# Kernel tuning notes

Measured on AMD Instinct MI355X. Metric: run time of the kernel, lower is better.

## Reference

```python
import jax, jax.numpy as jnp
import numpy as np


def setup_inputs() -> dict:
    key = jax.random.key(0)
    k1, k2, k3, k4, k5 = jax.random.split(key, 5)
    B, C, G, H, W = 2, 64, 4, 64, 64
    CG = C * G            # 256 complex input channels (flattened)
    DQK = max(C // 8, 1)  # 8  query/key channels after gabor pooling
    scale = 1.0 / np.sqrt(CG)
    x = jax.random.normal(k1, (2, B, C, G, H, W), dtype=jnp.float32)
    wq = jax.random.normal(k2, (2, DQK, CG), dtype=jnp.float32) * scale
    wk = jax.random.normal(k3, (2, DQK, CG), dtype=jnp.float32) * scale
    wv = jax.random.normal(k4, (2, CG, CG), dtype=jnp.float32) * scale
    gamma = jax.random.normal(k5, (1,), dtype=jnp.float32) * 0.1
    return {"x": x, "wq": wq, "wk": wk, "wv": wv, "gamma": gamma}


def _cconv1x1(w, xr, xi):
    """Complex 1x1 conv: (wr+i wi)(xr+i xi). w: (2,O,Cin), x: (B,Cin,L)."""
    wr, wi = w[0], w[1]
    yr = jnp.einsum('oc,bcl->bol', wr, xr) - jnp.einsum('oc,bcl->bol', wi, xi)
    yi = jnp.einsum('oc,bcl->bol', wr, xi) + jnp.einsum('oc,bcl->bol', wi, xr)
    return yr, yi


def reference(x, wq, wk, wv, gamma):
    _, B, C, G, H, W = x.shape
    L = H * W
    xr = x[0].reshape(B, C * G, L)
    xi = x[1].reshape(B, C * G, L)
    # complex Q (B,d,L) / K (B,d,L)
    qr, qi = _cconv1x1(wq, xr, xi)
    kr, ki = _cconv1x1(wk, xr, xi)
    # energy = Q^H-free complex bmm: energy[b,l,m] = sum_d q[b,d,l] * k[b,d,m]
    er = jnp.einsum('bdl,bdm->blm', qr, kr) - jnp.einsum('bdl,bdm->blm', qi, ki)
    ei = jnp.einsum('bdl,bdm->blm', qr, ki) + jnp.einsum('bdl,bdm->blm', qi, kr)
    # magnitude-squared softmax over last axis -> real attention (B,L,L)
    att = jax.nn.softmax(er * er + ei * ei, axis=-1)
    # complex V (B,CG,L); out[b,c,m] = sum_l v[b,c,l] * att[b,m,l]
    vr, vi = _cconv1x1(wv, xr, xi)
    out_r = jnp.einsum('bcl,bml->bcm', vr, att)
    out_i = jnp.einsum('bcl,bml->bcm', vi, att)
    out = jnp.stack([out_r, out_i]).reshape(2, B, C, G, H, W)
    return gamma * out + x
```

## Files before the change

### kernel.cpp

```cpp
#include <hip/hip_runtime.h>
#include <cstdint>

constexpr int Bc  = 2;
constexpr int CGc = 256;
constexpr int Dc  = 8;
constexpr int Lc  = 4096;

typedef __attribute__((ext_vector_type(8))) short short8;
typedef __attribute__((ext_vector_type(4))) float floatx4;

__device__ inline unsigned short f2bf(float f) {
  union { float f; unsigned u; } v; v.f = f;
  unsigned r = v.u + 0x7fffu + ((v.u >> 16) & 1u);
  return (unsigned short)(r >> 16);
}
__device__ inline float bf2f(unsigned short h) {
  return __uint_as_float((unsigned)h << 16);
}

__global__ __launch_bounds__(256) void init_wcat(float* __restrict__ stats,
                                                 const float* __restrict__ wv,
                                                 unsigned short* __restrict__ Wcat) {
  const int bx = blockIdx.x;
  if (bx < 64) {
    stats[bx * 256 + threadIdx.x] = 0.f;
    return;
  }
  const int i  = (bx - 64) * 256 + threadIdx.x;
  const int cc = i >> 9, k = i & 511;
  const int co = cc >> 8, c = cc & 255, ci = k >> 8, cin = k & 255;
  const float wr = wv[(size_t)c * CGc + cin];
  const float wi = wv[(size_t)(CGc + c) * CGc + cin];
  const float val = co == 0 ? (ci == 0 ? wr : -wi) : (ci == 0 ? wi : wr);
  Wcat[i] = f2bf(val);
}

__global__ __launch_bounds__(256) void xT_pack(const float* __restrict__ x,
                                               unsigned short* __restrict__ Xlk) {
  __shared__ float xs[64][65];
  const int tid = threadIdx.x;
  const int b   = blockIdx.z;
  const int l0  = blockIdx.x * 64;
  const int c0  = blockIdx.y * 64;
  const int lt  = tid & 63, r4 = tid >> 6;
#pragma unroll
  for (int p = 0; p < 16; ++p) {
    const int row  = p * 4 + r4;
    const int cin2 = c0 + row;
    const int comp = cin2 >> 8, cin = cin2 & 255;
    xs[row][lt] = x[((size_t)(comp * Bc + b) * CGc + cin) * Lc + l0 + lt];
  }
  __syncthreads();
#pragma unroll
  for (int p = 0; p < 16; ++p) {
    const int lr = p * 4 + r4;
    Xlk[((size_t)b * Lc + l0 + lr) * 512 + c0 + lt] = f2bf(xs[lt][lr]);
  }
}

__global__ __launch_bounds__(256) void qk_projpack(const float* __restrict__ x,
                                                   const float* __restrict__ wq,
                                                   const float* __restrict__ wk,
                                                   unsigned short* __restrict__ Qcat,
                                                   unsigned short* __restrict__ K1hi,
                                                   unsigned short* __restrict__ K1lo,
                                                   unsigned short* __restrict__ K2hi,
                                                   unsigned short* __restrict__ K2lo) {
  __shared__ float ws[4 * Dc * CGc];
  __shared__ float qs[32][16];
  __shared__ float ks[32][16];
  const int tid = threadIdx.x;
  const int b   = blockIdx.y;
  for (int i = tid; i < 2 * Dc * CGc; i += 256) {
    ws[i]                 = wq[i];
    ws[2 * Dc * CGc + i]  = wk[i];
  }
  __syncthreads();
  const int d  = tid >> 5;
  const int ml = tid & 31;
  const int m  = blockIdx.x * 32 + ml;
  const float* xr = x + ((size_t)(0 * Bc + b) * CGc) * Lc + m;
  const float* xi = x + ((size_t)(1 * Bc + b) * CGc) * Lc + m;
  const float* wqr = ws + d * CGc;
  const float* wqi = ws + (Dc + d) * CGc;
  const float* wkr = ws + 2 * Dc * CGc + d * CGc;
  const float* wki = ws + 2 * Dc * CGc + (Dc + d) * CGc;
  float qer = 0.f, qei = 0.f, ker = 0.f, kei = 0.f;
#pragma unroll 4
  for (int cin = 0; cin < CGc; ++cin) {
    const float vr = xr[(size_t)cin * Lc];
    const float vi = xi[(size_t)cin * Lc];
    const float a1 = wqr[cin], b1 = wqi[cin];
    qer = fmaf(a1, vr, qer); qer = fmaf(-b1, vi, qer);
    qei = fmaf(a1, vi, qei); qei = fmaf(b1, vr, qei);
    const float a2 = wkr[cin], b2 = wki[cin];
    ker = fmaf(a2, vr, ker); ker = fmaf(-b2, vi, ker);
    kei = fmaf(a2, vi, kei); kei = fmaf(b2, vr, kei);
  }
  qs[ml][d] = qer;  qs[ml][8 + d] = qei;
  ks[ml][d] = ker;  ks[ml][8 + d] = kei;
  __syncthreads();
  const int part = tid >> 5;
  const int rl   = tid & 31;
  const size_t r = (size_t)b * Lc + blockIdx.x * 32 + rl;
  if (part < 2) {
    unsigned u[8];
#pragma unroll
    for (int t = 0; t < 8; ++t) {
      const float v0 = qs[rl][2 * t], v1 = qs[rl][2 * t + 1];
      const unsigned short h0 = f2bf(v0), h1 = f2bf(v1);
      if (part == 0) {
        u[t] = (unsigned)h0 | ((unsigned)h1 << 16);
      } else {
        const unsigned short l0 = f2bf(v0 - bf2f(h0));
        const unsigned short l1 = f2bf(v1 - bf2f(h1));
        u[t] = (unsigned)l0 | ((unsigned)l1 << 16);
      }
    }
    uint4* dst = (uint4*)(Qcat + r * 32 + part * 16);
    dst[0] = make_uint4(u[0], u[1], u[2], u[3]);
    dst[1] = make_uint4(u[4], u[5], u[6], u[7]);
  } else if (part < 6) {
    float kv[16];
    if (part < 4) {
#pragma unroll
      for (int e = 0; e < 8; ++e) { kv[e] = ks[rl][e]; kv[8 + e] = -ks[rl][8 + e]; }
    } else {
#pragma unroll
      for (int e = 0; e < 8; ++e) { kv[e] = ks[rl][8 + e]; kv[8 + e] = ks[rl][e]; }
    }
    const int lo = part & 1;
    unsigned u[8];
#pragma unroll
    for (int t = 0; t < 8; ++t) {
      const unsigned short h0 = f2bf(kv[2 * t]), h1 = f2bf(kv[2 * t + 1]);
      if (!lo) {
        u[t] = (unsigned)h0 | ((unsigned)h1 << 16);
      } else {
        const unsigned short l0 = f2bf(kv[2 * t] - bf2f(h0));
        const unsigned short l1 = f2bf(kv[2 * t + 1] - bf2f(h1));
        u[t] = (unsigned)l0 | ((unsigned)l1 << 16);
      }
    }
    unsigned short* base = part < 4 ? (lo ? K1lo : K1hi) : (lo ? K2lo : K2hi);
    uint4* dst = (uint4*)(base + r * 16);
    dst[0] = make_uint4(u[0], u[1], u[2], u[3]);
    dst[1] = make_uint4(u[4], u[5], u[6], u[7]);
  }
}

__global__ __launch_bounds__(256) void v_gemm(const unsigned short* __restrict__ Wcat,
                                              const unsigned short* __restrict__ Xlk,
                                              unsigned short* __restrict__ vbf) {
  __shared__ short As[128 * 64];
  __shared__ short Bs[64 * 64];
  const int tid  = threadIdx.x;
  const int b    = blockIdx.z;
  const int cc0  = blockIdx.x * 128;
  const int l0   = blockIdx.y * 64;
  const int wid  = tid >> 6, lane = tid & 63;
  const int wcc  = (wid >> 1) * 64;
  const int wl   = (wid & 1) * 32;
  const int lrow = lane & 15, quad = lane >> 4;
  floatx4 acc[4][2] = {};
  const unsigned short* wsrc = Wcat + (size_t)cc0 * 512;
  const unsigned short* xsrc = Xlk + ((size_t)b * Lc + l0) * 512;
  int s_off[4], g_off[4];
#pragma unroll
  for (int r = 0; r < 4; ++r) {
    const int idx = r * 256 + tid;
    const int row = idx >> 3, ch = idx & 7;
    s_off[r] = row * 64 + (ch ^ (row & 7)) * 8;
    g_off[r] = row * 512 + ch * 8;
  }
  short8 ar[4], br[2];
#pragma unroll
  for (int r = 0; r < 4; ++r) ar[r] = *(const short8*)(wsrc + g_off[r]);
#pragma unroll
  for (int r = 0; r < 2; ++r) br[r] = *(const short8*)(xsrc + g_off[r]);
  for (int k0 = 0; k0 < 512; k0 += 64) {
    __syncthreads();
#pragma unroll
    for (int r = 0; r < 4; ++r) *(short8*)&As[s_off[r]] = ar[r];
#pragma unroll
    for (int r = 0; r < 2; ++r) *(short8*)&Bs[s_off[r]] = br[r];
    __syncthreads();
    if (k0 + 64 < 512) {
#pragma unroll
      for (int r = 0; r < 4; ++r) ar[r] = *(const short8*)(wsrc + g_off[r] + k0 + 64);
#pragma unroll
      for (int r = 0; r < 2; ++r) br[r] = *(const short8*)(xsrc + g_off[r] + k0 + 64);
    }
#pragma unroll
    for (int kk = 0; kk < 64; kk += 32) {
      const int cb = kk >> 3;
      short8 af[4], bf[2];
#pragma unroll
      for (int i = 0; i < 4; ++i)
        af[i] = *(const short8*)&As[(wcc + i * 16 + lrow) * 64 +
                                    ((cb + quad) ^ (lrow & 7)) * 8];
#pragma unroll
      for (int j = 0; j < 2; ++j)
        bf[j] = *(const short8*)&Bs[(wl + j * 16 + lrow) * 64 +
                                    ((cb + quad) ^ (lrow & 7)) * 8];
#pragma unroll
      for (int i = 0; i < 4; ++i)
#pragma unroll
        for (int j = 0; j < 2; ++j)
          acc[i][j] = __builtin_amdgcn_mfma_f32_16x16x32_bf16(af[i], bf[j], acc[i][j], 0, 0, 0);
    }
  }
#pragma unroll
  for (int i = 0; i < 4; ++i) {
    const int ccb = cc0 + wcc + i * 16 + quad * 4;
#pragma unroll
    for (int j = 0; j < 2; ++j) {
      const int l = l0 + wl + j * 16 + lrow;
#pragma unroll
      for (int rg = 0; rg < 4; ++rg)
        vbf[((size_t)b * 512 + ccb + rg) * Lc + l] = f2bf(acc[i][j][rg]);
    }
  }
}

__global__ __launch_bounds__(256) void e_max(const unsigned short* __restrict__ Qcat,
                                             const unsigned short* __restrict__ K1hi,
                                             const unsigned short* __restrict__ K2hi,
                                             float* __restrict__ Mrow) {
  const int tid  = threadIdx.x;
  const int w    = tid >> 6, lane = tid & 63;
  const int lrow = lane & 15, quad = lane >> 4, qsel = quad & 1;
  const int b    = blockIdx.z;
  const int m16  = blockIdx.x * 64 + w * 16;
  const int lbeg = blockIdx.y * 512;
  const size_t kb = (size_t)b * Lc;
  const short8 afrag = *(const short8*)(Qcat + (kb + m16 + lrow) * 32 + quad * 8);
  float mx[4] = {0.f, 0.f, 0.f, 0.f};
  for (int l0 = lbeg; l0 < lbeg + 512; l0 += 16) {
    const size_t l = kb + l0 + lrow;
    const short8 b1h = *(const short8*)(K1hi + l * 16 + qsel * 8);
    const short8 b2h = *(const short8*)(K2hi + l * 16 + qsel * 8);
    const floatx4 er = __builtin_amdgcn_mfma_f32_16x16x32_bf16(afrag, b1h, (floatx4){0.f, 0.f, 0.f, 0.f}, 0, 0, 0);
    const floatx4 ei = __builtin_amdgcn_mfma_f32_16x16x32_bf16(afrag, b2h, (floatx4){0.f, 0.f, 0.f, 0.f}, 0, 0, 0);
#pragma unroll
    for (int r = 0; r < 4; ++r) {
      float e = er[r] * er[r];
      e = fmaf(ei[r], ei[r], e);
      mx[r] = fmaxf(mx[r], e);
    }
  }
#pragma unroll
  for (int r = 0; r < 4; ++r) {
    float v = mx[r];
#pragma unroll
    for (int off = 1; off < 16; off <<= 1) v = fmaxf(v, __shfl_xor(v, off));
    if (lrow == 0)
      atomicMax((unsigned*)&Mrow[kb + m16 + quad * 4 + r], __float_as_uint(v));
  }
}

__global__ __launch_bounds__(256) void e_exp(const unsigned short* __restrict__ Qcat,
                                             const unsigned short* __restrict__ K1hi,
                                             const unsigned short* __restrict__ K1lo,
                                             const unsigned short* __restrict__ K2hi,
                                             const unsigned short* __restrict__ K2lo,
                                             const float* __restrict__ Mrow,
                                             unsigned short* __restrict__ att,
                                             float* __restrict__ Ssum) {
  const int tid  = threadIdx.x;
  const int w    = tid >> 6, lane = tid & 63;
  const int lrow = lane & 15, quad = lane >> 4, qsel = quad & 1;
  const int b    = blockIdx.z;
  const int m16  = blockIdx.x * 64 + w * 16;
  const int lbeg = blockIdx.y * 512;
  const size_t kb = (size_t)b * Lc;
  const short8 afrag = *(const short8*)(Qcat + (kb + m16 + lrow) * 32 + quad * 8);
  float Mv[4], sum[4] = {};
#pragma unroll
  for (int r = 0; r < 4; ++r) Mv[r] = Mrow[kb + m16 + quad * 4 + r];
  for (int l0 = lbeg; l0 < lbeg + 512; l0 += 16) {
    const size_t l = kb + l0 + lrow;
    const short8 b1h = *(const short8*)(K1hi + l * 16 + qsel * 8);
    const short8 b1l = *(const short8*)(K1lo + l * 16 + qsel * 8);
    const short8 b2h = *(const short8*)(K2hi + l * 16 + qsel * 8);
    const short8 b2l = *(const short8*)(K2lo + l * 16 + qsel * 8);
    floatx4 er = __builtin_amdgcn_mfma_f32_16x16x32_bf16(afrag, b1l, (floatx4){0.f, 0.f, 0.f, 0.f}, 0, 0, 0);
    er = __builtin_amdgcn_mfma_f32_16x16x32_bf16(afrag, b1h, er, 0, 0, 0);
    floatx4 ei = __builtin_amdgcn_mfma_f32_16x16x32_bf16(afrag, b2l, (floatx4){0.f, 0.f, 0.f, 0.f}, 0, 0, 0);
    ei = __builtin_amdgcn_mfma_f32_16x16x32_bf16(afrag, b2h, ei, 0, 0, 0);
#pragma unroll
    for (int r = 0; r < 4; ++r) {
      float e = er[r] * er[r];
      e = fmaf(ei[r], ei[r], e);
      const float wgt = __expf(e - Mv[r]);
      sum[r] += wgt;
      att[(kb + m16 + quad * 4 + r) * Lc + l0 + lrow] = f2bf(wgt);
    }
  }
#pragma unroll
  for (int r = 0; r < 4; ++r) {
    float v = sum[r];
#pragma unroll
    for (int off = 1; off < 16; off <<= 1) v += __shfl_xor(v, off);
    if (lrow == 0) atomicAdd(&Ssum[kb + m16 + quad * 4 + r], v);
  }
}

__device__ __forceinline__ void pv_stage(const unsigned short* __restrict__ vsrc,
                                         const unsigned short* __restrict__ asrc,
                                         short* lds_buf, int k0, int wid, int lane) {
  const int rsub = lane >> 3;
  const int ch   = (lane & 7) ^ rsub;
#pragma unroll
  for (int t = 0; t < 4; ++t) {
    const int q    = wid * 4 + t;
    const int tile = q >> 4;
    const int j    = q & 15;
    const int row  = j * 8 + rsub;
    const unsigned short* g =
        (tile == 0 ? vsrc : asrc) + (size_t)row * Lc + k0 + ch * 8;
    short* l = lds_buf + tile * 8192 + j * 512;
    __builtin_amdgcn_global_load_lds(
        (const __attribute__((address_space(1))) void*)g,
        (__attribute__((address_space(3))) void*)l, 16, 0, 0);
  }
}

__device__ __forceinline__ void pv_compute32(const short* __restrict__ As,
                                             const short* __restrict__ Bs,
                                             int cb, int wcc, int wm, int lrow, int quad,
                                             floatx4 (&acc)[4][4]) {
  short8 af[4], bf[4];
#pragma unroll
  for (int i = 0; i < 4; ++i)
    af[i] = *(const short8*)&As[(wcc + i * 16 + lrow) * 64 +
                                ((cb + quad) ^ (lrow & 7)) * 8];
#pragma unroll
  for (int j = 0; j < 4; ++j)
    bf[j] = *(const short8*)&Bs[(wm + j * 16 + lrow) * 64 +
                                ((cb + quad) ^ (lrow & 7)) * 8];
#pragma unroll
  for (int i = 0; i < 4; ++i)
#pragma unroll
    for (int j = 0; j < 4; ++j)
      acc[i][j] = __builtin_amdgcn_mfma_f32_16x16x32_bf16(af[i], bf[j], acc[i][j], 0, 0, 0);
}

__global__ __launch_bounds__(512, 2) void pv_gemm(const unsigned short* __restrict__ v,
                                                  const unsigned short* __restrict__ att,
                                                  const float* __restrict__ Ssum,
                                                  const float* __restrict__ x,
                                                  const float* __restrict__ gamma,
                                                  float* __restrict__ out) {
  extern __shared__ short smem[];
  const int flat = blockIdx.x;
  const int swz  = (flat & 7) * 32 + (flat >> 3);
  const int b    = swz >> 7;
  const int rem  = swz & 127;
  const int m0   = (rem >> 2) * 128;
  const int cc0  = (rem & 3) * 128;
  const int tid  = threadIdx.x;
  const int wid  = tid >> 6, lane = tid & 63;
  const int g    = wid >> 2;
  const int w4   = wid & 3;
  const int wcc  = (w4 >> 1) * 64;
  const int wm   = (w4 & 1) * 64;
  const int lrow = lane & 15, quad = lane >> 4;
  const int cb   = g * 4;
  floatx4 acc[4][4] = {};
  const unsigned short* vsrc = v   + ((size_t)b * 512 + cc0) * Lc;
  const unsigned short* asrc = att + ((size_t)b * Lc + m0) * Lc;
  pv_stage(vsrc, asrc, smem,          0, wid, lane);
  pv_stage(vsrc, asrc, smem + 16384, 64, wid, lane);
  int cur = 0;
  for (int p = 0; p < 64; ++p) {
    if (p < 63) {
      asm volatile("s_waitcnt vmcnt(4)" ::: "memory");
    } else {
      asm volatile("s_waitcnt vmcnt(0)" ::: "memory");
    }
    __builtin_amdgcn_s_barrier();
    __builtin_amdgcn_sched_barrier(0);
    if (p + 2 < 64) {
      const int nxt = cur + 2 > 2 ? cur - 1 : cur + 2;
      pv_stage(vsrc, asrc, smem + nxt * 16384, (p + 2) * 64, wid, lane);
    }
    __builtin_amdgcn_sched_barrier(0);
    pv_compute32(smem + cur * 16384, smem + cur * 16384 + 8192,
                 cb, wcc, wm, lrow, quad, acc);
    __builtin_amdgcn_sched_barrier(0);
    cur = cur + 1 > 2 ? 0 : cur + 1;
  }
  __syncthreads();
  float* red = (float*)smem;
  if (g == 1) {
#pragma unroll
    for (int i = 0; i < 4; ++i)
#pragma unroll
      for (int j = 0; j < 4; ++j) {
        const int tq = i * 4 + j;
        *(floatx4*)&red[((w4 * 64 + lane) * 16 + (tq ^ (lane & 15))) * 4] = acc[i][j];
      }
  }
  __syncthreads();
  if (g == 0) {
#pragma unroll
    for (int i = 0; i < 4; ++i)
#pragma unroll
      for (int j = 0; j < 4; ++j) {
        const int tq = i * 4 + j;
        const floatx4 o = *(const floatx4*)&red[((w4 * 64 + lane) * 16 + (tq ^ (lane & 15))) * 4];
        acc[i][j] += o;
      }
    const float gm = gamma[0];
    float svj[4];
#pragma unroll
    for (int j = 0; j < 4; ++j)
      svj[j] = gm / Ssum[(size_t)b * Lc + m0 + wm + j * 16 + lrow];
#pragma unroll
    for (int i = 0; i < 4; ++i) {
      const int ccb = cc0 + wcc + i * 16 + quad * 4;
#pragma unroll
      for (int j = 0; j < 4; ++j) {
        const int m = m0 + wm + j * 16 + lrow;
#pragma unroll
        for (int rg = 0; rg < 4; ++rg) {
          const int cc   = ccb + rg;
          const int comp = cc >> 8, c = cc & 255;
          const size_t idx = (((size_t)comp * Bc + b) * CGc + c) * Lc + m;
          out[idx] = svj[j] * acc[i][j][rg] + x[idx];
        }
      }
    }
  }
}

extern "C" void kernel_launch(void* const* d_in, const int* in_sizes, int n_in,
                              void* d_out, int out_size, void* d_ws, size_t ws_size,
                              hipStream_t stream) {
  const float* x     = (const float*)d_in[0];
  const float* wq    = (const float*)d_in[1];
  const float* wk    = (const float*)d_in[2];
  const float* wv    = (const float*)d_in[3];
  const float* gamma = (const float*)d_in[4];
  float* out = (float*)d_out;

  float* q    = (float*)d_ws;
  float* kk   = q    + (size_t)Bc * Lc * 16;
  float* Mrow = kk   + (size_t)Bc * Lc * 16;
  float* Ssum = Mrow + (size_t)Bc * Lc;
  unsigned short* vbf  = (unsigned short*)(Ssum + (size_t)Bc * Lc);
  unsigned short* att  = vbf + (size_t)Bc * 512 * Lc;
  unsigned short* Xlk  = att;
  unsigned short* Qcat = att + (size_t)Bc * Lc * Lc;
  unsigned short* K1hi = Qcat + (size_t)Bc * Lc * 32;
  unsigned short* K1lo = K1hi + (size_t)Bc * Lc * 16;
  unsigned short* K2hi = K1lo + (size_t)Bc * Lc * 16;
  unsigned short* K2lo = K2hi + (size_t)Bc * Lc * 16;
  unsigned short* Wcat = K2lo + (size_t)Bc * Lc * 16;

  init_wcat<<<dim3(64 + 1024), 256, 0, stream>>>(Mrow, wv, Wcat);
  qk_projpack<<<dim3(Lc / 32, Bc), 256, 0, stream>>>(x, wq, wk, Qcat, K1hi, K1lo, K2hi, K2lo);
  xT_pack<<<dim3(Lc / 64, 8, Bc), 256, 0, stream>>>(x, Xlk);
  v_gemm<<<dim3(512 / 128, Lc / 64, Bc), 256, 0, stream>>>(Wcat, Xlk, vbf);
  e_max<<<dim3(Lc / 64, 8, Bc), 256, 0, stream>>>(Qcat, K1hi, K2hi, Mrow);
  e_exp<<<dim3(Lc / 64, 8, Bc), 256, 0, stream>>>(Qcat, K1hi, K1lo, K2hi, K2lo, Mrow, att, Ssum);
  pv_gemm<<<dim3(256), 512, 3 * 16384 * sizeof(short), stream>>>(vbf, att, Ssum, x, gamma, out);
}
```

Measured before the change: 194.6 us.

## Fuse row-max and exp passes in one block; widen PV GEMM K-tile and split-K

Merges the e_max and e_exp kernels into one 1024-thread kernel where each block owns 32 rows across all L. The row max and row sum are reduced in LDS instead of through global atomics, which removes the stats-zeroing pass and one launch. The PV GEMM moves to 1024 threads per block with 128-wide K tiles and double buffering instead of triple buffering with 64-wide tiles. It also gains a 4-way split-K reduction through LDS. In exchange, occupancy drops to one block per CU and there is less prefetch depth to hide load latency.

```diff
diff --git a/kernel.cpp b/kernel.cpp
--- a/kernel.cpp
+++ b/kernel.cpp
@@ -18,15 +18,9 @@
   return __uint_as_float((unsigned)h << 16);
 }
 
-__global__ __launch_bounds__(256) void init_wcat(float* __restrict__ stats,
-                                                 const float* __restrict__ wv,
+__global__ __launch_bounds__(256) void wcat_pack(const float* __restrict__ wv,
                                                  unsigned short* __restrict__ Wcat) {
-  const int bx = blockIdx.x;
-  if (bx < 64) {
-    stats[bx * 256 + threadIdx.x] = 0.f;
-    return;
-  }
-  const int i  = (bx - 64) * 256 + threadIdx.x;
+  const int i  = blockIdx.x * 256 + threadIdx.x;
   const int cc = i >> 9, k = i & 511;
   const int co = cc >> 8, c = cc & 255, ci = k >> 8, cin = k & 255;
   const float wr = wv[(size_t)c * CGc + cin];
@@ -223,17 +217,26 @@
   }
 }
 
-__global__ __launch_bounds__(256) void e_max(const unsigned short* __restrict__ Qcat,
-                                             const unsigned short* __restrict__ K1hi,
-                                             const unsigned short* __restrict__ K2hi,
-                                             float* __restrict__ Mrow) {
+__global__ __launch_bounds__(1024) void emax_exp(const unsigned short* __restrict__ Qcat,
+                                                 const unsigned short* __restrict__ K1hi,
+                                                 const unsigned short* __restrict__ K1lo,
+                                                 const unsigned short* __restrict__ K2hi,
+                                                 const unsigned short* __restrict__ K2lo,
+                                                 unsigned short* __restrict__ att,
+                                                 float* __restrict__ Ssum) {
+  __shared__ unsigned maxb[32];
+  __shared__ float    sumb[32];
   const int tid  = threadIdx.x;
-  const int w    = tid >> 6, lane = tid & 63;
+  const int wv   = tid >> 6, lane = tid & 63;
   const int lrow = lane & 15, quad = lane >> 4, qsel = quad & 1;
-  const int b    = blockIdx.z;
-  const int m16  = blockIdx.x * 64 + w * 16;
-  const int lbeg = blockIdx.y * 512;
+  const int b    = blockIdx.y;
+  const int rg   = wv & 1;
+  const int sl   = wv >> 1;
+  const int m16  = blockIdx.x * 32 + rg * 16;
+  const int lbeg = sl * 512;
   const size_t kb = (size_t)b * Lc;
+  if (tid < 32) { maxb[tid] = 0u; sumb[tid] = 0.f; }
+  __syncthreads();
   const short8 afrag = *(const short8*)(Qcat + (kb + m16 + lrow) * 32 + quad * 8);
   float mx[4] = {0.f, 0.f, 0.f, 0.f};
   for (int l0 = lbeg; l0 < lbeg + 512; l0 += 16) {
@@ -255,29 +258,12 @@
 #pragma unroll
     for (int off = 1; off < 16; off <<= 1) v = fmaxf(v, __shfl_xor(v, off));
     if (lrow == 0)
-      atomicMax((unsigned*)&Mrow[kb + m16 + quad * 4 + r], __float_as_uint(v));
-  }
-}
-
-__global__ __launch_bounds__(256) void e_exp(const unsigned short* __restrict__ Qcat,
-                                             const unsigned short* __restrict__ K1hi,
-                                             const unsigned short* __restrict__ K1lo,
-                                             const unsigned short* __restrict__ K2hi,
-                                             const unsigned short* __restrict__ K2lo,
-                                             const float* __restrict__ Mrow,
-                                             unsigned short* __restrict__ att,
-                                             float* __restrict__ Ssum) {
-  const int tid  = threadIdx.x;
-  const int w    = tid >> 6, lane = tid & 63;
-  const int lrow = lane & 15, quad = lane >> 4, qsel = quad & 1;
-  const int b    = blockIdx.z;
-  const int m16  = blockIdx.x * 64 + w * 16;
-  const int lbeg = blockIdx.y * 512;
-  const size_t kb = (size_t)b * Lc;
-  const short8 afrag = *(const short8*)(Qcat + (kb + m16 + lrow) * 32 + quad * 8);
+      atomicMax(&maxb[rg * 16 + quad * 4 + r], __float_as_uint(v));
+  }
+  __syncthreads();
   float Mv[4], sum[4] = {};
 #pragma unroll
-  for (int r = 0; r < 4; ++r) Mv[r] = Mrow[kb + m16 + quad * 4 + r];
+  for (int r = 0; r < 4; ++r) Mv[r] = __uint_as_float(maxb[rg * 16 + quad * 4 + r]);
   for (int l0 = lbeg; l0 < lbeg + 512; l0 += 16) {
     const size_t l = kb + l0 + lrow;
     const short8 b1h = *(const short8*)(K1hi + l * 16 + qsel * 8);
@@ -302,42 +288,45 @@
     float v = sum[r];
 #pragma unroll
     for (int off = 1; off < 16; off <<= 1) v += __shfl_xor(v, off);
-    if (lrow == 0) atomicAdd(&Ssum[kb + m16 + quad * 4 + r], v);
-  }
-}
-
-__device__ __forceinline__ void pv_stage(const unsigned short* __restrict__ vsrc,
-                                         const unsigned short* __restrict__ asrc,
-                                         short* lds_buf, int k0, int wid, int lane) {
-  const int rsub = lane >> 3;
-  const int ch   = (lane & 7) ^ rsub;
+    if (lrow == 0) atomicAdd(&sumb[rg * 16 + quad * 4 + r], v);
+  }
+  __syncthreads();
+  if (tid < 32) Ssum[kb + blockIdx.x * 32 + tid] = sumb[tid];
+}
+
+__device__ __forceinline__ void pv_stage128(const unsigned short* __restrict__ vsrc,
+                                            const unsigned short* __restrict__ asrc,
+                                            short* lds_buf, int k0, int wid, int lane) {
+  const int rsub = lane >> 4;
+  const int cs   = lane & 15;
 #pragma unroll
   for (int t = 0; t < 4; ++t) {
     const int q    = wid * 4 + t;
-    const int tile = q >> 4;
-    const int j    = q & 15;
-    const int row  = j * 8 + rsub;
+    const int tile = q >> 5;
+    const int j    = q & 31;
+    const int row  = j * 4 + rsub;
+    const int gch  = cs ^ (row & 7);
     const unsigned short* g =
-        (tile == 0 ? vsrc : asrc) + (size_t)row * Lc + k0 + ch * 8;
-    short* l = lds_buf + tile * 8192 + j * 512;
+        (tile == 0 ? vsrc : asrc) + (size_t)row * Lc + k0 + gch * 8;
+    short* l = lds_buf + tile * 16384 + j * 512;
     __builtin_amdgcn_global_load_lds(
         (const __attribute__((address_space(1))) void*)g,
         (__attribute__((address_space(3))) void*)l, 16, 0, 0);
   }
 }
 
-__device__ __forceinline__ void pv_compute32(const short* __restrict__ As,
-                                             const short* __restrict__ Bs,
-                                             int cb, int wcc, int wm, int lrow, int quad,
-                                             floatx4 (&acc)[4][4]) {
+__device__ __forceinline__ void pv_compute128(const short* __restrict__ As,
+                                              const short* __restrict__ Bs,
+                                              int cb, int wcc, int wm, int lrow, int quad,
+                                              floatx4 (&acc)[4][4]) {
   short8 af[4], bf[4];
 #pragma unroll
   for (int i = 0; i < 4; ++i)
-    af[i] = *(const short8*)&As[(wcc + i * 16 + lrow) * 64 +
+    af[i] = *(const short8*)&As[(wcc + i * 16 + lrow) * 128 +
                                 ((cb + quad) ^ (lrow & 7)) * 8];
 #pragma unroll
   for (int j = 0; j < 4; ++j)
-    bf[j] = *(const short8*)&Bs[(wm + j * 16 + lrow) * 64 +
+    bf[j] = *(const short8*)&Bs[(wm + j * 16 + lrow) * 128 +
                                 ((cb + quad) ^ (lrow & 7)) * 8];
 #pragma unroll
   for (int i = 0; i < 4; ++i)
@@ -346,12 +335,12 @@
       acc[i][j] = __builtin_amdgcn_mfma_f32_16x16x32_bf16(af[i], bf[j], acc[i][j], 0, 0, 0);
 }
 
-__global__ __launch_bounds__(512, 2) void pv_gemm(const unsigned short* __restrict__ v,
-                                                  const unsigned short* __restrict__ att,
-                                                  const float* __restrict__ Ssum,
-                                                  const float* __restrict__ x,
-                                                  const float* __restrict__ gamma,
-                                                  float* __restrict__ out) {
+__global__ __launch_bounds__(1024, 1) void pv_gemm(const unsigned short* __restrict__ v,
+                                                   const unsigned short* __restrict__ att,
+                                                   const float* __restrict__ Ssum,
+                                                   const float* __restrict__ x,
+                                                   const float* __restrict__ gamma,
+                                                   float* __restrict__ out) {
   extern __shared__ short smem[];
   const int flat = blockIdx.x;
   const int swz  = (flat & 7) * 32 + (flat >> 3);
@@ -370,30 +359,44 @@
   floatx4 acc[4][4] = {};
   const unsigned short* vsrc = v   + ((size_t)b * 512 + cc0) * Lc;
   const unsigned short* asrc = att + ((size_t)b * Lc + m0) * Lc;
-  pv_stage(vsrc, asrc, smem,          0, wid, lane);
-  pv_stage(vsrc, asrc, smem + 16384, 64, wid, lane);
-  int cur = 0;
-  for (int p = 0; p < 64; ++p) {
-    if (p < 63) {
-      asm volatile("s_waitcnt vmcnt(4)" ::: "memory");
-    } else {
-      asm volatile("s_waitcnt vmcnt(0)" ::: "memory");
-    }
+  pv_stage128(vsrc, asrc, smem, 0, wid, lane);
+  for (int p = 0; p < 32; ++p) {
+    asm volatile("s_waitcnt vmcnt(0)" ::: "memory");
     __builtin_amdgcn_s_barrier();
     __builtin_amdgcn_sched_barrier(0);
-    if (p + 2 < 64) {
-      const int nxt = cur + 2 > 2 ? cur - 1 : cur + 2;
-      pv_stage(vsrc, asrc, smem + nxt * 16384, (p + 2) * 64, wid, lane);
-    }
+    if (p + 1 < 32)
+      pv_stage128(vsrc, asrc, smem + ((p + 1) & 1) * 32768, (p + 1) * 128, wid, lane);
     __builtin_amdgcn_sched_barrier(0);
-    pv_compute32(smem + cur * 16384, smem + cur * 16384 + 8192,
-                 cb, wcc, wm, lrow, quad, acc);
+    pv_compute128(smem + (p & 1) * 32768, smem + (p & 1) * 32768 + 16384,
+                  cb, wcc, wm, lrow, quad, acc);
     __builtin_amdgcn_sched_barrier(0);
-    cur = cur + 1 > 2 ? 0 : cur + 1;
   }
   __syncthreads();
   float* red = (float*)smem;
-  if (g == 1) {
+  if (g == 1 || g == 3) {
+    float* dst = red + (g == 3 ? 16384 : 0);
+#pragma unroll
+    for (int i = 0; i < 4; ++i)
+#pragma unroll
+      for (int j = 0; j < 4; ++j) {
+        const int tq = i * 4 + j;
+        *(floatx4*)&dst[((w4 * 64 + lane) * 16 + (tq ^ (lane & 15))) * 4] = acc[i][j];
+      }
+  }
+  __syncthreads();
+  if (g == 0 || g == 2) {
+    const float* src = red + (g == 2 ? 16384 : 0);
+#pragma unroll
+    for (int i = 0; i < 4; ++i)
+#pragma unroll
+      for (int j = 0; j < 4; ++j) {
+        const int tq = i * 4 + j;
+        const floatx4 o = *(const floatx4*)&src[((w4 * 64 + lane) * 16 + (tq ^ (lane & 15))) * 4];
+        acc[i][j] += o;
+      }
+  }
+  __syncthreads();
+  if (g == 2) {
 #pragma unroll
     for (int i = 0; i < 4; ++i)
 #pragma unroll
@@ -459,11 +462,10 @@
   unsigned short* K2lo = K2hi + (size_t)Bc * Lc * 16;
   unsigned short* Wcat = K2lo + (size_t)Bc * Lc * 16;
 
-  init_wcat<<<dim3(64 + 1024), 256, 0, stream>>>(Mrow, wv, Wcat);
+  wcat_pack<<<dim3((512 * 512) / 256), 256, 0, stream>>>(wv, Wcat);
   qk_projpack<<<dim3(Lc / 32, Bc), 256, 0, stream>>>(x, wq, wk, Qcat, K1hi, K1lo, K2hi, K2lo);
   xT_pack<<<dim3(Lc / 64, 8, Bc), 256, 0, stream>>>(x, Xlk);
   v_gemm<<<dim3(512 / 128, Lc / 64, Bc), 256, 0, stream>>>(Wcat, Xlk, vbf);
-  e_max<<<dim3(Lc / 64, 8, Bc), 256, 0, stream>>>(Qcat, K1hi, K2hi, Mrow);
-  e_exp<<<dim3(Lc / 64, 8, Bc), 256, 0, stream>>>(Qcat, K1hi, K1lo, K2hi, K2lo, Mrow, att, Ssum);
-  pv_gemm<<<dim3(256), 512, 3 * 16384 * sizeof(short), stream>>>(vbf, att, Ssum, x, gamma, out);
-}
+  emax_exp<<<dim3(Lc / 32, Bc), 1024, 0, stream>>>(Qcat, K1hi, K1lo, K2hi, K2lo, att, Ssum);
+  pv_gemm<<<dim3(256), 1024, 2 * 32768 * sizeof(short), stream>>>(vbf, att, Ssum, x, gamma, out);
+}
```

After: 191.1 us. Within noise of the previous version (-1.8%).
